# Performance work log

Hardware: AMD Instinct MI355X
Metric: run time of the kernel (lower is better)

Reference implementation:

```python
import jax, jax.numpy as jnp
import numpy as np

N_FEATURES = 512
D_MODEL = 1024
BATCH = 256
LN_EPS = 1e-5


def setup_inputs() -> dict:
    key = jax.random.key(0)
    ks = jax.random.split(key, 8)
    x = jax.random.normal(ks[0], (BATCH, N_FEATURES), dtype=jnp.float32)
    prev_ca = jax.random.uniform(ks[1], (BATCH, D_MODEL), dtype=jnp.float32)
    # phase_proj: Linear(n_features, d_model)
    Wp = jax.random.normal(ks[2], (D_MODEL, N_FEATURES), dtype=jnp.float32) * (1.0 / np.sqrt(N_FEATURES))
    bp = jnp.zeros((D_MODEL,), dtype=jnp.float32)
    # ca_gate: Linear(d_model, d_model//2) + sigmoid
    Wg = jax.random.normal(ks[3], (D_MODEL // 2, D_MODEL), dtype=jnp.float32) * (1.0 / np.sqrt(D_MODEL))
    bg = jnp.zeros((D_MODEL // 2,), dtype=jnp.float32)
    # coupling matrix W (learned param, prev_W is None in default path)
    W = jax.random.normal(ks[4], (D_MODEL, D_MODEL), dtype=jnp.float32) * 0.01
    # LayerNorm params
    gamma = jnp.ones((D_MODEL,), dtype=jnp.float32)
    beta = jnp.zeros((D_MODEL,), dtype=jnp.float32)
    return {"x": x, "prev_ca": prev_ca, "Wp": Wp, "bp": bp, "Wg": Wg, "bg": bg, "W": W, "gamma": gamma, "beta": beta}


def _layernorm(h, gamma, beta):
    mu = jnp.mean(h, axis=-1, keepdims=True)
    var = jnp.mean(jnp.square(h - mu), axis=-1, keepdims=True)
    return (h - mu) * jax.lax.rsqrt(var + LN_EPS) * gamma + beta


def reference(x, prev_ca, Wp, bp, Wg, bg, W, gamma, beta):
    # phi: [B, d]
    phi = x @ Wp.T + bp
    # pairwise phase coherence |cos(phi_i - phi_j)| -> mean over j: [B, d]
    coherence = jnp.abs(jnp.cos(phi[:, :, None] - phi[:, None, :]))  # [B, d, d]
    ca_update = jnp.mean(coherence, axis=2)
    ca = prev_ca * 0.95 + ca_update * 0.05
    # calcium gate: sigmoid(Linear(d -> d//2)), tiled to d
    ca_gate = jax.nn.sigmoid(ca @ Wg.T + bg)  # [B, d//2]
    coupled = phi @ W  # [B, d]
    ca_gate_full = jnp.concatenate([ca_gate, ca_gate], axis=1)  # [B, d]
    features = coupled * ca_gate_full
    features = _layernorm(features + phi, gamma, beta)
    return features, ca, W
```

## Files before the change

### kernel.cpp

```cpp
#include <hip/hip_runtime.h>
#include <math.h>

#define BATCH   256
#define NFEAT   512
#define DMODEL  1024
#define DHALF   512
#define LN_EPS  1e-5f
#define LDSK    68
#define LDSN    132

typedef float f2 __attribute__((ext_vector_type(2)));
typedef float f4 __attribute__((ext_vector_type(4)));

template <int M, int N, int K, int SPLIT, bool B_NT, bool BIAS, bool SIG>
__device__ __forceinline__ void gemm_tile128(
    const float* __restrict__ A, const float* __restrict__ B,
    const float* __restrict__ bias, float* __restrict__ Cp,
    float* __restrict__ As, float* __restrict__ Bs,
    const int bx, const int by, const int z, const int tid) {
  constexpr int KC = K / SPLIT;
  constexpr int NT = KC / 64;
  const int bm = bx * 64, bn = by * 128, kb = z * KC;
  const int tx  = tid & 15;
  const int ty  = tid >> 4;
  const int c4  = tid & 15;
  const int r16 = tid >> 4;
  const int c8  = tid & 31;
  const int r8  = tid >> 5;

  f4 ar[4], br[8];

  auto load_tile = [&](int t) {
#pragma unroll
    for (int jj = 0; jj < 4; ++jj)
      ar[jj] = *(const f4*)(
          &A[(size_t)(bm + r16 + jj * 16) * K + kb + t * 64 + c4 * 4]);
    if (B_NT) {
#pragma unroll
      for (int jj = 0; jj < 8; ++jj)
        br[jj] = *(const f4*)(
            &B[(size_t)(bn + r16 + jj * 16) * K + kb + t * 64 + c4 * 4]);
    } else {
#pragma unroll
      for (int jj = 0; jj < 8; ++jj)
        br[jj] = *(const f4*)(
            &B[(size_t)(kb + t * 64 + r8 + jj * 8) * N + bn + c8 * 4]);
    }
  };
  auto store_tile = [&]() {
#pragma unroll
    for (int jj = 0; jj < 4; ++jj) {
#pragma unroll
      for (int j = 0; j < 4; ++j) {
        const int kk = c4 * 4 + j;
        const int m  = r16 + jj * 16;
        As[kk * LDSK + ((((m >> 2) ^ c4) << 2) | (m & 3))] = ar[jj][j];
      }
    }
    if (B_NT) {
#pragma unroll
      for (int jj = 0; jj < 8; ++jj) {
#pragma unroll
        for (int j = 0; j < 4; ++j) {
          const int kk = c4 * 4 + j;
          const int n  = r16 + jj * 16;
          Bs[kk * LDSN + ((((n >> 2) ^ c4) << 2) | (n & 3))] = br[jj][j];
        }
      }
    } else {
#pragma unroll
      for (int jj = 0; jj < 8; ++jj) {
        const int kk = r8 + jj * 8;
        *(f4*)(&Bs[kk * LDSN + ((c8 ^ ((kk >> 2) & 15)) << 2)]) = br[jj];
      }
    }
  };

  f2 acc[4][4];
#pragma unroll
  for (int i = 0; i < 4; ++i)
#pragma unroll
    for (int p = 0; p < 4; ++p) acc[i][p] = (f2)0.f;

  load_tile(0);
  store_tile();
  __syncthreads();

  for (int t = 0; t < NT; ++t) {
    if (t + 1 < NT) load_tile(t + 1);
#pragma unroll
    for (int kk = 0; kk < 64; ++kk) {
      const int gk = (kk >> 2) & 15;
      const f4 af  = *(const f4*)(&As[kk * LDSK + ((ty ^ gk) << 2)]);
      const f4 bf0 = *(const f4*)(&Bs[kk * LDSN + (((2 * tx) ^ gk) << 2)]);
      const f4 bf1 = *(const f4*)(&Bs[kk * LDSN + (((2 * tx + 1) ^ gk) << 2)]);
      const f2 b[4] = {{bf0.x, bf0.y}, {bf0.z, bf0.w},
                       {bf1.x, bf1.y}, {bf1.z, bf1.w}};
#pragma unroll
      for (int i = 0; i < 4; ++i) {
        const f2 ai = {af[i], af[i]};
#pragma unroll
        for (int p = 0; p < 4; ++p) acc[i][p] += ai * b[p];
      }
    }
    if (t + 1 < NT) {
      __syncthreads();
      store_tile();
      __syncthreads();
    }
  }

  f4 bv0 = {0.f, 0.f, 0.f, 0.f}, bv1 = bv0;
  if (BIAS && SPLIT == 1) {
    bv0 = *(const f4*)(&bias[bn + tx * 8]);
    bv1 = *(const f4*)(&bias[bn + tx * 8 + 4]);
  }
#pragma unroll
  for (int i = 0; i < 4; ++i) {
    const int m = bm + ty * 4 + i;
    f4 c0 = {acc[i][0].x, acc[i][0].y, acc[i][1].x, acc[i][1].y};
    f4 c1 = {acc[i][2].x, acc[i][2].y, acc[i][3].x, acc[i][3].y};
    if (SPLIT == 1) {
      if (BIAS) { c0 += bv0; c1 += bv1; }
      if (SIG) {
#pragma unroll
        for (int u = 0; u < 4; ++u) {
          c0[u] = 1.f / (1.f + expf(-c0[u]));
          c1[u] = 1.f / (1.f + expf(-c1[u]));
        }
      }
      *(f4*)(&Cp[(size_t)m * N + bn + tx * 8]) = c0;
      *(f4*)(&Cp[(size_t)m * N + bn + tx * 8 + 4]) = c1;
    } else {
      *(f4*)(&Cp[((size_t)z * M + m) * N + bn + tx * 8]) = c0;
      *(f4*)(&Cp[((size_t)z * M + m) * N + bn + tx * 8 + 4]) = c1;
    }
  }
}

template <int PARTS, bool WRITE_PHI>
__device__ __forceinline__ void coherence_row(
    const float* __restrict__ parts, const float* __restrict__ bp,
    const float* __restrict__ prev_ca, float* __restrict__ phi_out,
    float* __restrict__ ca_out, float* __restrict__ cc, float* __restrict__ ss,
    const int b, const int tid) {
  f4 ph = ((const f4*)(parts + (size_t)b * DMODEL))[tid];
  if (PARTS > 1) {
#pragma unroll
    for (int z = 1; z < PARTS; ++z)
      ph += ((const f4*)(parts + ((size_t)z * BATCH + b) * DMODEL))[tid];
    ph += ((const f4*)bp)[tid];
    if (WRITE_PHI) ((f4*)(phi_out + (size_t)b * DMODEL))[tid] = ph;
  }
  float ci[4], si[4];
#pragma unroll
  for (int u = 0; u < 4; ++u) { si[u] = __sinf(ph[u]); ci[u] = __cosf(ph[u]); }
  *(f4*)(&cc[tid * 4]) = f4{ci[0], ci[1], ci[2], ci[3]};
  *(f4*)(&ss[tid * 4]) = f4{si[0], si[1], si[2], si[3]};
  __syncthreads();

  float accA[4] = {0.f, 0.f, 0.f, 0.f};
  float accB[4] = {0.f, 0.f, 0.f, 0.f};
#pragma unroll 4
  for (int j4 = 0; j4 < DMODEL; j4 += 4) {
    const f4 cy = *(const f4*)(&cc[j4]);
    const f4 sy = *(const f4*)(&ss[j4]);
    const f2 cy01 = {cy.x, cy.y}, cy23 = {cy.z, cy.w};
    const f2 sy01 = {sy.x, sy.y}, sy23 = {sy.z, sy.w};
#pragma unroll
    for (int u = 0; u < 4; ++u) {
      const f2 cu = {ci[u], ci[u]};
      const f2 su = {si[u], si[u]};
      f2 t = su * sy01; t = cu * cy01 + t;
      accA[u] += __builtin_fabsf(t.x);
      accB[u] += __builtin_fabsf(t.y);
      t = su * sy23; t = cu * cy23 + t;
      accA[u] += __builtin_fabsf(t.x);
      accB[u] += __builtin_fabsf(t.y);
    }
  }
  const f4 pc = ((const f4*)(prev_ca + (size_t)b * DMODEL))[tid];
  f4 o;
#pragma unroll
  for (int u = 0; u < 4; ++u)
    o[u] = pc[u] * 0.95f + (accA[u] + accB[u]) * (0.05f / (float)DMODEL);
  ((f4*)(ca_out + (size_t)b * DMODEL))[tid] = o;
}

template <int PCP, int PGP, bool GATE_RAW>
__device__ __forceinline__ void ln_row(
    const float* __restrict__ pC, const float* __restrict__ pG,
    const float* __restrict__ phi, const float* __restrict__ bg,
    const float* __restrict__ gamma, const float* __restrict__ beta,
    float* __restrict__ out, float* __restrict__ red, const int b,
    const int tid) {
  float gs[2];
#pragma unroll
  for (int h = 0; h < 2; ++h) {
    const int gi = tid + h * 256;
    float s = 0.f;
#pragma unroll
    for (int z = 0; z < PGP; ++z)
      s += pG[((size_t)z * BATCH + b) * DHALF + gi];
    if (GATE_RAW) {
      s += bg[gi];
      s = 1.f / (1.f + expf(-s));
    }
    gs[h] = s;
  }
  float hv[4];
  float sum = 0.f, sumsq = 0.f;
#pragma unroll
  for (int u = 0; u < 4; ++u) {
    const int n = tid + u * 256;
    float cpl = 0.f;
#pragma unroll
    for (int z = 0; z < PCP; ++z)
      cpl += pC[((size_t)z * BATCH + b) * DMODEL + n];
    const float v = fmaf(cpl, gs[u & 1], phi[(size_t)b * DMODEL + n]);
    hv[u] = v;
    sum += v;
    sumsq = fmaf(v, v, sumsq);
  }
  const int lane = tid & 63;
  const int wid  = tid >> 6;
#pragma unroll
  for (int off = 32; off > 0; off >>= 1) {
    sum   += __shfl_down(sum, off);
    sumsq += __shfl_down(sumsq, off);
  }
  if (lane == 0) { red[wid] = sum; red[4 + wid] = sumsq; }
  __syncthreads();
  sum   = red[0] + red[1] + red[2] + red[3];
  sumsq = red[4] + red[5] + red[6] + red[7];
  const float mu   = sum * (1.f / DMODEL);
  const float var  = sumsq * (1.f / DMODEL) - mu * mu;
  const float rstd = rsqrtf(var + LN_EPS);
#pragma unroll
  for (int u = 0; u < 4; ++u) {
    const int n = tid + u * 256;
    out[(size_t)b * DMODEL + n] = (hv[u] - mu) * rstd * gamma[n] + beta[n];
  }
}

__global__ __launch_bounds__(256, 2) void k_phi_wcopy(
    const float* __restrict__ x, const float* __restrict__ Wp,
    float* __restrict__ pbuf, const f4* __restrict__ wsrc,
    f4* __restrict__ wdst) {
  __shared__ __align__(16) float As[64 * LDSK];
  __shared__ __align__(16) float Bs[64 * LDSN];
  const int gb = blockIdx.x, tid = threadIdx.x;
  if (gb < 256) {
    gemm_tile128<BATCH, DMODEL, NFEAT, 8, true, false, false>(
        x, Wp, nullptr, pbuf, As, Bs, gb & 3, (gb >> 2) & 7, gb >> 5, tid);
  } else {
    const int base = (gb - 256) * 8192 + tid;
#pragma unroll
    for (int k = 0; k < 32; ++k) wdst[base + k * 256] = wsrc[base + k * 256];
  }
}

__global__ __launch_bounds__(256, 2) void k_coherence(
    const float* __restrict__ pbuf, const float* __restrict__ bp,
    const float* __restrict__ prev_ca, float* __restrict__ phi,
    float* __restrict__ ca_out) {
  __shared__ __align__(16) float lds[2 * DMODEL];
  coherence_row<8, true>(pbuf, bp, prev_ca, phi, ca_out, lds, lds + DMODEL,
                         blockIdx.x, threadIdx.x);
}

__global__ __launch_bounds__(256, 2) void k_gate_coupled(
    const float* __restrict__ ca, const float* __restrict__ Wg,
    const float* __restrict__ phi, const float* __restrict__ W,
    float* __restrict__ pG, float* __restrict__ pC) {
  __shared__ __align__(16) float As[64 * LDSK];
  __shared__ __align__(16) float Bs[64 * LDSN];
  const int gb = blockIdx.x, tid = threadIdx.x;
  if (gb < 256) {
    gemm_tile128<BATCH, DHALF, DMODEL, 16, true, false, false>(
        ca, Wg, nullptr, pG, As, Bs, gb & 3, (gb >> 2) & 3, gb >> 4, tid);
  } else {
    const int g2 = gb - 256;
    gemm_tile128<BATCH, DMODEL, DMODEL, 8, false, false, false>(
        phi, W, nullptr, pC, As, Bs, g2 & 3, (g2 >> 2) & 7, g2 >> 5, tid);
  }
}

__global__ __launch_bounds__(256, 2) void k_ln(
    const float* __restrict__ pC, const float* __restrict__ pG,
    const float* __restrict__ phi, const float* __restrict__ bg,
    const float* __restrict__ gamma, const float* __restrict__ beta,
    float* __restrict__ out) {
  __shared__ float red[8];
  ln_row<8, 16, true>(pC, pG, phi, bg, gamma, beta, out, red, blockIdx.x,
                      threadIdx.x);
}

template <int M, int N, int K, bool B_NT, bool BIAS, bool SIG>
__global__ __launch_bounds__(256, 2) void k_gemm1(
    const float* __restrict__ A, const float* __restrict__ B,
    const float* __restrict__ bias, float* __restrict__ C) {
  __shared__ __align__(16) float As[64 * LDSK];
  __shared__ __align__(16) float Bs[64 * LDSN];
  gemm_tile128<M, N, K, 1, B_NT, BIAS, SIG>(A, B, bias, C, As, Bs,
                                            blockIdx.x, blockIdx.y, 0,
                                            threadIdx.x);
}

__global__ __launch_bounds__(256, 2) void k_coherence1(
    const float* __restrict__ phi, const float* __restrict__ prev_ca,
    float* __restrict__ ca_out) {
  __shared__ __align__(16) float lds[2 * DMODEL];
  coherence_row<1, false>(phi, nullptr, prev_ca, nullptr, ca_out, lds,
                          lds + DMODEL, blockIdx.x, threadIdx.x);
}

__global__ __launch_bounds__(256, 2) void k_ln1(
    const float* __restrict__ pC, const float* __restrict__ pG,
    const float* __restrict__ phi, const float* __restrict__ bg,
    const float* __restrict__ gamma, const float* __restrict__ beta,
    float* __restrict__ out) {
  __shared__ float red[8];
  ln_row<1, 1, false>(pC, pG, phi, bg, gamma, beta, out, red, blockIdx.x,
                      threadIdx.x);
}

extern "C" void kernel_launch(void* const* d_in, const int* in_sizes, int n_in,
                              void* d_out, int out_size, void* d_ws,
                              size_t ws_size, hipStream_t stream) {
  const float* x       = (const float*)d_in[0];
  const float* prev_ca = (const float*)d_in[1];
  const float* Wp      = (const float*)d_in[2];
  const float* bp      = (const float*)d_in[3];
  const float* Wg      = (const float*)d_in[4];
  const float* bg      = (const float*)d_in[5];
  const float* W       = (const float*)d_in[6];
  const float* gamma   = (const float*)d_in[7];
  const float* beta    = (const float*)d_in[8];

  float* out_features = (float*)d_out;
  float* out_ca       = out_features + BATCH * DMODEL;
  float* out_W        = out_ca + BATCH * DMODEL;

  float* phi  = (float*)d_ws;
  float* pbuf = phi + BATCH * DMODEL;
  float* pG   = pbuf + 8 * BATCH * DMODEL;
  float* pC   = pG + 16 * BATCH * DHALF;

  const size_t need_main =
      (size_t)(BATCH * DMODEL + 8 * BATCH * DMODEL + 16 * BATCH * DHALF +
               8 * BATCH * DMODEL) * sizeof(float);
  const size_t need_compact =
      (size_t)(2 * BATCH * DMODEL + BATCH * DHALF) * sizeof(float);

  if (ws_size >= need_main) {
    k_phi_wcopy<<<288, 256, 0, stream>>>(x, Wp, pbuf, (const f4*)W,
                                         (f4*)out_W);
    k_coherence<<<256, 256, 0, stream>>>(pbuf, bp, prev_ca, phi, out_ca);
    k_gate_coupled<<<512, 256, 0, stream>>>(out_ca, Wg, phi, W, pG, pC);
    k_ln<<<256, 256, 0, stream>>>(pC, pG, phi, bg, gamma, beta, out_features);
  } else {
    float* scratch = (ws_size >= need_compact) ? (float*)d_ws : out_W;
    float* sphi    = scratch;
    float* gate    = sphi + BATCH * DMODEL;
    float* coupled = gate + BATCH * DHALF;
    k_gemm1<BATCH, DMODEL, NFEAT, true, true, false>
        <<<dim3(4, 8), 256, 0, stream>>>(x, Wp, bp, sphi);
    k_coherence1<<<256, 256, 0, stream>>>(sphi, prev_ca, out_ca);
    k_gemm1<BATCH, DHALF, DMODEL, true, true, true>
        <<<dim3(4, 4), 256, 0, stream>>>(out_ca, Wg, bg, gate);
    k_gemm1<BATCH, DMODEL, DMODEL, false, false, false>
        <<<dim3(4, 8), 256, 0, stream>>>(sphi, W, nullptr, coupled);
    k_ln1<<<256, 256, 0, stream>>>(coupled, gate, sphi, bg, gamma, beta,
                                   out_features);
    hipMemcpyAsync(out_W, W, (size_t)DMODEL * DMODEL * sizeof(float),
                   hipMemcpyDeviceToDevice, stream);
  }
}
```

Baseline: 132.7 us.

## Shrink GEMM tiles to 64x64 and raise split-K to increase block count

Replaces the 64x128 GEMM tile with a 64x64 tile that uses unpadded 64-wide LDS rows and halves the per-thread accumulators. Grid sizes double for all GEMMs, and the coupled GEMM moves from split-K 8 to 16. Launch bounds rise to 4 blocks per SIMD to fill the GPU with more waves. The layernorm row is also vectorised to f4 loads and stores. The cost is twice as many partial-sum buffers to write and reduce in the LN kernel, lower per-thread arithmetic intensity, and possible LDS bank conflicts now that padding is gone.

```diff
diff --git a/kernel.cpp b/kernel.cpp
--- a/kernel.cpp
+++ b/kernel.cpp
@@ -6,81 +6,62 @@
 #define DMODEL  1024
 #define DHALF   512
 #define LN_EPS  1e-5f
-#define LDSK    68
-#define LDSN    132
 
 typedef float f2 __attribute__((ext_vector_type(2)));
 typedef float f4 __attribute__((ext_vector_type(4)));
 
 template <int M, int N, int K, int SPLIT, bool B_NT, bool BIAS, bool SIG>
-__device__ __forceinline__ void gemm_tile128(
+__device__ __forceinline__ void gemm_tile64(
     const float* __restrict__ A, const float* __restrict__ B,
     const float* __restrict__ bias, float* __restrict__ Cp,
     float* __restrict__ As, float* __restrict__ Bs,
     const int bx, const int by, const int z, const int tid) {
   constexpr int KC = K / SPLIT;
   constexpr int NT = KC / 64;
-  const int bm = bx * 64, bn = by * 128, kb = z * KC;
+  const int bm = bx * 64, bn = by * 64, kb = z * KC;
   const int tx  = tid & 15;
   const int ty  = tid >> 4;
   const int c4  = tid & 15;
   const int r16 = tid >> 4;
-  const int c8  = tid & 31;
-  const int r8  = tid >> 5;
-
-  f4 ar[4], br[8];
+
+  f4 ar[4], br[4];
 
   auto load_tile = [&](int t) {
 #pragma unroll
-    for (int jj = 0; jj < 4; ++jj)
-      ar[jj] = *(const f4*)(
-          &A[(size_t)(bm + r16 + jj * 16) * K + kb + t * 64 + c4 * 4]);
-    if (B_NT) {
-#pragma unroll
-      for (int jj = 0; jj < 8; ++jj)
-        br[jj] = *(const f4*)(
-            &B[(size_t)(bn + r16 + jj * 16) * K + kb + t * 64 + c4 * 4]);
-    } else {
-#pragma unroll
-      for (int jj = 0; jj < 8; ++jj)
-        br[jj] = *(const f4*)(
-            &B[(size_t)(kb + t * 64 + r8 + jj * 8) * N + bn + c8 * 4]);
+    for (int jj = 0; jj < 4; ++jj) {
+      const int row = r16 + jj * 16;
+      ar[jj] = *(const f4*)(&A[(size_t)(bm + row) * K + kb + t * 64 + c4 * 4]);
+      if (B_NT)
+        br[jj] = *(const f4*)(&B[(size_t)(bn + row) * K + kb + t * 64 + c4 * 4]);
+      else
+        br[jj] = *(const f4*)(&B[(size_t)(kb + t * 64 + row) * N + bn + c4 * 4]);
     }
   };
   auto store_tile = [&]() {
 #pragma unroll
     for (int jj = 0; jj < 4; ++jj) {
+      const int m = r16 + jj * 16;
 #pragma unroll
       for (int j = 0; j < 4; ++j) {
         const int kk = c4 * 4 + j;
-        const int m  = r16 + jj * 16;
-        As[kk * LDSK + ((((m >> 2) ^ c4) << 2) | (m & 3))] = ar[jj][j];
+        As[kk * 64 + ((((m >> 2) ^ c4) << 2) | (m & 3))] = ar[jj][j];
       }
-    }
-    if (B_NT) {
-#pragma unroll
-      for (int jj = 0; jj < 8; ++jj) {
+      if (B_NT) {
 #pragma unroll
         for (int j = 0; j < 4; ++j) {
           const int kk = c4 * 4 + j;
-          const int n  = r16 + jj * 16;
-          Bs[kk * LDSN + ((((n >> 2) ^ c4) << 2) | (n & 3))] = br[jj][j];
+          Bs[kk * 64 + ((((m >> 2) ^ c4) << 2) | (m & 3))] = br[jj][j];
         }
+      } else {
+        const int kk = m;
+        *(f4*)(&Bs[kk * 64 + ((c4 ^ ((kk >> 2) & 15)) << 2)]) = br[jj];
       }
-    } else {
-#pragma unroll
-      for (int jj = 0; jj < 8; ++jj) {
-        const int kk = r8 + jj * 8;
-        *(f4*)(&Bs[kk * LDSN + ((c8 ^ ((kk >> 2) & 15)) << 2)]) = br[jj];
-      }
     }
   };
 
-  f2 acc[4][4];
-#pragma unroll
-  for (int i = 0; i < 4; ++i)
-#pragma unroll
-    for (int p = 0; p < 4; ++p) acc[i][p] = (f2)0.f;
+  f2 acc[4][2];
+#pragma unroll
+  for (int i = 0; i < 4; ++i) { acc[i][0] = (f2)0.f; acc[i][1] = (f2)0.f; }
 
   load_tile(0);
   store_tile();
@@ -91,16 +72,15 @@
 #pragma unroll
     for (int kk = 0; kk < 64; ++kk) {
       const int gk = (kk >> 2) & 15;
-      const f4 af  = *(const f4*)(&As[kk * LDSK + ((ty ^ gk) << 2)]);
-      const f4 bf0 = *(const f4*)(&Bs[kk * LDSN + (((2 * tx) ^ gk) << 2)]);
-      const f4 bf1 = *(const f4*)(&Bs[kk * LDSN + (((2 * tx + 1) ^ gk) << 2)]);
-      const f2 b[4] = {{bf0.x, bf0.y}, {bf0.z, bf0.w},
-                       {bf1.x, bf1.y}, {bf1.z, bf1.w}};
+      const f4 af = *(const f4*)(&As[kk * 64 + ((ty ^ gk) << 2)]);
+      const f4 bf = *(const f4*)(&Bs[kk * 64 + ((tx ^ gk) << 2)]);
+      const f2 b01 = {bf.x, bf.y};
+      const f2 b23 = {bf.z, bf.w};
 #pragma unroll
       for (int i = 0; i < 4; ++i) {
         const f2 ai = {af[i], af[i]};
-#pragma unroll
-        for (int p = 0; p < 4; ++p) acc[i][p] += ai * b[p];
+        acc[i][0] += ai * b01;
+        acc[i][1] += ai * b23;
       }
     }
     if (t + 1 < NT) {
@@ -110,30 +90,21 @@
     }
   }
 
-  f4 bv0 = {0.f, 0.f, 0.f, 0.f}, bv1 = bv0;
-  if (BIAS && SPLIT == 1) {
-    bv0 = *(const f4*)(&bias[bn + tx * 8]);
-    bv1 = *(const f4*)(&bias[bn + tx * 8 + 4]);
-  }
+  f4 bv = {0.f, 0.f, 0.f, 0.f};
+  if (BIAS && SPLIT == 1) bv = *(const f4*)(&bias[bn + tx * 4]);
 #pragma unroll
   for (int i = 0; i < 4; ++i) {
     const int m = bm + ty * 4 + i;
-    f4 c0 = {acc[i][0].x, acc[i][0].y, acc[i][1].x, acc[i][1].y};
-    f4 c1 = {acc[i][2].x, acc[i][2].y, acc[i][3].x, acc[i][3].y};
+    f4 cv = {acc[i][0].x, acc[i][0].y, acc[i][1].x, acc[i][1].y};
     if (SPLIT == 1) {
-      if (BIAS) { c0 += bv0; c1 += bv1; }
+      if (BIAS) cv += bv;
       if (SIG) {
 #pragma unroll
-        for (int u = 0; u < 4; ++u) {
-          c0[u] = 1.f / (1.f + expf(-c0[u]));
-          c1[u] = 1.f / (1.f + expf(-c1[u]));
-        }
+        for (int u = 0; u < 4; ++u) cv[u] = 1.f / (1.f + expf(-cv[u]));
       }
-      *(f4*)(&Cp[(size_t)m * N + bn + tx * 8]) = c0;
-      *(f4*)(&Cp[(size_t)m * N + bn + tx * 8 + 4]) = c1;
+      *(f4*)(&Cp[(size_t)m * N + bn + tx * 4]) = cv;
     } else {
-      *(f4*)(&Cp[((size_t)z * M + m) * N + bn + tx * 8]) = c0;
-      *(f4*)(&Cp[((size_t)z * M + m) * N + bn + tx * 8 + 4]) = c1;
+      *(f4*)(&Cp[((size_t)z * M + m) * N + bn + tx * 4]) = cv;
     }
   }
 }
@@ -194,34 +165,25 @@
     const float* __restrict__ gamma, const float* __restrict__ beta,
     float* __restrict__ out, float* __restrict__ red, const int b,
     const int tid) {
-  float gs[2];
-#pragma unroll
-  for (int h = 0; h < 2; ++h) {
-    const int gi = tid + h * 256;
-    float s = 0.f;
-#pragma unroll
-    for (int z = 0; z < PGP; ++z)
-      s += pG[((size_t)z * BATCH + b) * DHALF + gi];
-    if (GATE_RAW) {
-      s += bg[gi];
-      s = 1.f / (1.f + expf(-s));
-    }
-    gs[h] = s;
-  }
-  float hv[4];
-  float sum = 0.f, sumsq = 0.f;
-#pragma unroll
-  for (int u = 0; u < 4; ++u) {
-    const int n = tid + u * 256;
-    float cpl = 0.f;
-#pragma unroll
-    for (int z = 0; z < PCP; ++z)
-      cpl += pC[((size_t)z * BATCH + b) * DMODEL + n];
-    const float v = fmaf(cpl, gs[u & 1], phi[(size_t)b * DMODEL + n]);
-    hv[u] = v;
-    sum += v;
-    sumsq = fmaf(v, v, sumsq);
-  }
+  const int gi = tid & 127;
+  f4 g = {0.f, 0.f, 0.f, 0.f};
+#pragma unroll
+  for (int z = 0; z < PGP; ++z)
+    g += ((const f4*)(pG + ((size_t)z * BATCH + b) * DHALF))[gi];
+  if (GATE_RAW) {
+    g += ((const f4*)bg)[gi];
+#pragma unroll
+    for (int u = 0; u < 4; ++u) g[u] = 1.f / (1.f + expf(-g[u]));
+  }
+  f4 cpl = {0.f, 0.f, 0.f, 0.f};
+#pragma unroll
+  for (int z = 0; z < PCP; ++z)
+    cpl += ((const f4*)(pC + ((size_t)z * BATCH + b) * DMODEL))[tid];
+  const f4 phv = ((const f4*)(phi + (size_t)b * DMODEL))[tid];
+  const f4 h = cpl * g + phv;
+
+  float sum   = h.x + h.y + h.z + h.w;
+  float sumsq = h.x * h.x + h.y * h.y + h.z * h.z + h.w * h.w;
   const int lane = tid & 63;
   const int wid  = tid >> 6;
 #pragma unroll
@@ -236,25 +198,26 @@
   const float mu   = sum * (1.f / DMODEL);
   const float var  = sumsq * (1.f / DMODEL) - mu * mu;
   const float rstd = rsqrtf(var + LN_EPS);
-#pragma unroll
-  for (int u = 0; u < 4; ++u) {
-    const int n = tid + u * 256;
-    out[(size_t)b * DMODEL + n] = (hv[u] - mu) * rstd * gamma[n] + beta[n];
-  }
-}
-
-__global__ __launch_bounds__(256, 2) void k_phi_wcopy(
+  const f4 gm = ((const f4*)gamma)[tid];
+  const f4 bt = ((const f4*)beta)[tid];
+  f4 o;
+#pragma unroll
+  for (int u = 0; u < 4; ++u) o[u] = (h[u] - mu) * rstd * gm[u] + bt[u];
+  ((f4*)(out + (size_t)b * DMODEL))[tid] = o;
+}
+
+__global__ __launch_bounds__(256, 4) void k_phi_wcopy(
     const float* __restrict__ x, const float* __restrict__ Wp,
     float* __restrict__ pbuf, const f4* __restrict__ wsrc,
     f4* __restrict__ wdst) {
-  __shared__ __align__(16) float As[64 * LDSK];
-  __shared__ __align__(16) float Bs[64 * LDSN];
+  __shared__ __align__(16) float As[64 * 64];
+  __shared__ __align__(16) float Bs[64 * 64];
   const int gb = blockIdx.x, tid = threadIdx.x;
-  if (gb < 256) {
-    gemm_tile128<BATCH, DMODEL, NFEAT, 8, true, false, false>(
-        x, Wp, nullptr, pbuf, As, Bs, gb & 3, (gb >> 2) & 7, gb >> 5, tid);
+  if (gb < 512) {
+    gemm_tile64<BATCH, DMODEL, NFEAT, 8, true, false, false>(
+        x, Wp, nullptr, pbuf, As, Bs, gb & 3, (gb >> 2) & 15, gb >> 6, tid);
   } else {
-    const int base = (gb - 256) * 8192 + tid;
+    const int base = (gb - 512) * 8192 + tid;
 #pragma unroll
     for (int k = 0; k < 32; ++k) wdst[base + k * 256] = wsrc[base + k * 256];
   }
@@ -269,42 +232,41 @@
                          blockIdx.x, threadIdx.x);
 }
 
-__global__ __launch_bounds__(256, 2) void k_gate_coupled(
+__global__ __launch_bounds__(256, 4) void k_gate_coupled(
     const float* __restrict__ ca, const float* __restrict__ Wg,
     const float* __restrict__ phi, const float* __restrict__ W,
     float* __restrict__ pG, float* __restrict__ pC) {
-  __shared__ __align__(16) float As[64 * LDSK];
-  __shared__ __align__(16) float Bs[64 * LDSN];
+  __shared__ __align__(16) float As[64 * 64];
+  __shared__ __align__(16) float Bs[64 * 64];
   const int gb = blockIdx.x, tid = threadIdx.x;
-  if (gb < 256) {
-    gemm_tile128<BATCH, DHALF, DMODEL, 16, true, false, false>(
-        ca, Wg, nullptr, pG, As, Bs, gb & 3, (gb >> 2) & 3, gb >> 4, tid);
+  if (gb < 512) {
+    gemm_tile64<BATCH, DHALF, DMODEL, 16, true, false, false>(
+        ca, Wg, nullptr, pG, As, Bs, gb & 3, (gb >> 2) & 7, gb >> 5, tid);
   } else {
-    const int g2 = gb - 256;
-    gemm_tile128<BATCH, DMODEL, DMODEL, 8, false, false, false>(
-        phi, W, nullptr, pC, As, Bs, g2 & 3, (g2 >> 2) & 7, g2 >> 5, tid);
-  }
-}
-
-__global__ __launch_bounds__(256, 2) void k_ln(
+    const int g2 = gb - 512;
+    gemm_tile64<BATCH, DMODEL, DMODEL, 16, false, false, false>(
+        phi, W, nullptr, pC, As, Bs, g2 & 3, (g2 >> 2) & 15, g2 >> 6, tid);
+  }
+}
+
+__global__ __launch_bounds__(256, 4) void k_ln(
     const float* __restrict__ pC, const float* __restrict__ pG,
     const float* __restrict__ phi, const float* __restrict__ bg,
     const float* __restrict__ gamma, const float* __restrict__ beta,
     float* __restrict__ out) {
   __shared__ float red[8];
-  ln_row<8, 16, true>(pC, pG, phi, bg, gamma, beta, out, red, blockIdx.x,
-                      threadIdx.x);
+  ln_row<16, 16, true>(pC, pG, phi, bg, gamma, beta, out, red, blockIdx.x,
+                       threadIdx.x);
 }
 
 template <int M, int N, int K, bool B_NT, bool BIAS, bool SIG>
-__global__ __launch_bounds__(256, 2) void k_gemm1(
+__global__ __launch_bounds__(256, 4) void k_gemm1(
     const float* __restrict__ A, const float* __restrict__ B,
     const float* __restrict__ bias, float* __restrict__ C) {
-  __shared__ __align__(16) float As[64 * LDSK];
-  __shared__ __align__(16) float Bs[64 * LDSN];
-  gemm_tile128<M, N, K, 1, B_NT, BIAS, SIG>(A, B, bias, C, As, Bs,
-                                            blockIdx.x, blockIdx.y, 0,
-                                            threadIdx.x);
+  __shared__ __align__(16) float As[64 * 64];
+  __shared__ __align__(16) float Bs[64 * 64];
+  gemm_tile64<M, N, K, 1, B_NT, BIAS, SIG>(A, B, bias, C, As, Bs, blockIdx.x,
+                                           blockIdx.y, 0, threadIdx.x);
 }
 
 __global__ __launch_bounds__(256, 2) void k_coherence1(
@@ -315,7 +277,7 @@
                           lds + DMODEL, blockIdx.x, threadIdx.x);
 }
 
-__global__ __launch_bounds__(256, 2) void k_ln1(
+__global__ __launch_bounds__(256, 4) void k_ln1(
     const float* __restrict__ pC, const float* __restrict__ pG,
     const float* __restrict__ phi, const float* __restrict__ bg,
     const float* __restrict__ gamma, const float* __restrict__ beta,
@@ -349,15 +311,15 @@
 
   const size_t need_main =
       (size_t)(BATCH * DMODEL + 8 * BATCH * DMODEL + 16 * BATCH * DHALF +
-               8 * BATCH * DMODEL) * sizeof(float);
+               16 * BATCH * DMODEL) * sizeof(float);
   const size_t need_compact =
       (size_t)(2 * BATCH * DMODEL + BATCH * DHALF) * sizeof(float);
 
   if (ws_size >= need_main) {
-    k_phi_wcopy<<<288, 256, 0, stream>>>(x, Wp, pbuf, (const f4*)W,
+    k_phi_wcopy<<<544, 256, 0, stream>>>(x, Wp, pbuf, (const f4*)W,
                                          (f4*)out_W);
     k_coherence<<<256, 256, 0, stream>>>(pbuf, bp, prev_ca, phi, out_ca);
-    k_gate_coupled<<<512, 256, 0, stream>>>(out_ca, Wg, phi, W, pG, pC);
+    k_gate_coupled<<<1536, 256, 0, stream>>>(out_ca, Wg, phi, W, pG, pC);
     k_ln<<<256, 256, 0, stream>>>(pC, pG, phi, bg, gamma, beta, out_features);
   } else {
     float* scratch = (ws_size >= need_compact) ? (float*)d_ws : out_W;
@@ -365,12 +327,12 @@
     float* gate    = sphi + BATCH * DMODEL;
     float* coupled = gate + BATCH * DHALF;
     k_gemm1<BATCH, DMODEL, NFEAT, true, true, false>
-        <<<dim3(4, 8), 256, 0, stream>>>(x, Wp, bp, sphi);
+        <<<dim3(4, 16), 256, 0, stream>>>(x, Wp, bp, sphi);
     k_coherence1<<<256, 256, 0, stream>>>(sphi, prev_ca, out_ca);
     k_gemm1<BATCH, DHALF, DMODEL, true, true, true>
-        <<<dim3(4, 4), 256, 0, stream>>>(out_ca, Wg, bg, gate);
+        <<<dim3(4, 8), 256, 0, stream>>>(out_ca, Wg, bg, gate);
     k_gemm1<BATCH, DMODEL, DMODEL, false, false, false>
-        <<<dim3(4, 8), 256, 0, stream>>>(sphi, W, nullptr, coupled);
+        <<<dim3(4, 16), 256, 0, stream>>>(sphi, W, nullptr, coupled);
     k_ln1<<<256, 256, 0, stream>>>(coupled, gate, sphi, bg, gamma, beta,
                                    out_features);
     hipMemcpyAsync(out_W, W, (size_t)DMODEL * DMODEL * sizeof(float),
```

New measurement: 126.5 us. -4.6%, faster.
